# Kernel optimization log

Measured on AMD Instinct MI355X. Metric: run time of the kernel, lower is better.

## Reference

```python
import jax, jax.numpy as jnp
import numpy as np

B, C, S = 4, 2, 4096          # batch, in_channels, samples
K, NK, OUT = 64, 32, 512      # kernel_size, num_kernels, out_channels


def setup_inputs() -> dict:
    key = jax.random.key(0)
    k1, k2, k3, k4 = jax.random.split(key, 4)
    x = jax.random.normal(k1, (B, C, S), dtype=jnp.float32)
    # LearnableSTFTFunction.learnable_weights: (num_kernels, kernel_size), torch.randn init
    stft_w = jax.random.normal(k2, (NK, K), dtype=jnp.float32)
    # Conv1d(in=C*K*NK, out=OUT, kernel=1): weight (OUT, C*K*NK), bias (OUT,)
    conv_w = jax.random.normal(k3, (OUT, C * K * NK), dtype=jnp.float32) * 0.02
    conv_b = jax.random.normal(k4, (OUT,), dtype=jnp.float32) * 0.02
    return {"x": x, "stft_w": stft_w, "conv_w": conv_w, "conv_b": conv_b}


def reference(x, stft_w, conv_w, conv_b):
    b, c, s = x.shape
    nk, k = stft_w.shape
    # F.pad(x, (0, K-1)) then unfold(-1, K, 1) -> (b, c, s, K) sliding windows
    xp = jnp.pad(x, ((0, 0), (0, 0), (0, k - 1)))
    idx = jnp.arange(s)[:, None] + jnp.arange(k)[None, :]  # (s, K)
    win = xp[:, :, idx]  # (b, c, s, K)
    # einsum('ijklm,lm->ijkml') with l=1 broadcast: elementwise per-kernel weighting,
    # no reduction over m -> (b, c, s, K, NK)
    xw = jnp.einsum('bcsm,lm->bcsml', win, stft_w)
    # torch raw reshape (row-major), deliberately mixing s into channel blocks
    xr = xw.reshape(b, c * k * nk, s)
    # 1x1 Conv1d == channel matmul, then ReLU
    out = jnp.einsum('bis,oi->bos', xr, conv_w) + conv_b[None, :, None]
    return jax.nn.relu(out)
```

## Files before the change

kernel.cpp:

```cpp
#include <hip/hip_runtime.h>
#include <hip/hip_bf16.h>

#define NB   4
#define NC   2
#define NS   4096
#define NOUT 512
#define UPAD 80

typedef short  short8_t  __attribute__((ext_vector_type(8)));
typedef short  short4_t  __attribute__((ext_vector_type(4)));
typedef float  float16_t __attribute__((ext_vector_type(16)));

__device__ __forceinline__ short bf16s(float f) {
    union { __hip_bfloat16 b; short s; } u;
    u.b = __float2bfloat16(f);
    return u.s;
}
__device__ __forceinline__ float s2f(unsigned short s) {
    union { unsigned int u; float f; } v;
    v.u = ((unsigned int)s) << 16;
    return v.f;
}

template<int KCN>
__global__ __launch_bounds__(256)
void gemm_partials(const float* __restrict__ x,
                   const float* __restrict__ conv_w,
                   unsigned short* __restrict__ hpart)
{
    constexpr int KC      = 4096 / KCN;
    constexpr int XSZ     = KC + 56;
    constexpr int ASTRIDE = KC + 8;
    static_assert(KCN >= 8, "A-tile LDS exceeds 160KB below KCN=8");

    __shared__ __align__(16) short aS[128 * ASTRIDE];
    __shared__ __align__(16) short xS[16][XSZ];

    const int blk = blockIdx.x;
    const int kc  = blk % KCN;
    const int ot  = (blk / KCN) & 3;
    const int b   = blk / (KCN * 4);

    const int K0 = kc * KC;
    const int c  = K0 >> 11;
    const int tb = K0 & 2047;
    const int tid = threadIdx.x;

    const float* xc = x + (size_t)(b * NC + c) * NS;
    for (int i = tid; i < XSZ; i += 256) {
        int ge = (tb + i) * 2;
        float fe = (ge     < NS) ? xc[ge]     : 0.0f;
        float fo = (ge + 1 < NS) ? xc[ge + 1] : 0.0f;
        short se = bf16s(fe), so = bf16s(fo);
        #pragma unroll
        for (int r = 0; r < 8; ++r) {
            int j = i - r;
            if (j >= 0) { xS[r][j] = se; xS[8 + r][j] = so; }
        }
    }

    {
        const int rr = tid >> 5;
        const int cc = (tid & 31) * 4;
        const float* wbase = conv_w + (size_t)(ot * 128) * 4096 + K0;
        #pragma unroll
        for (int cb = 0; cb < KC; cb += 128) {
            #pragma unroll
            for (int it = 0; it < 16; ++it) {
                int row = it * 8 + rr;
                float4 v = *(const float4*)(wbase + (size_t)row * 4096 + cb + cc);
                short4_t p = { bf16s(v.x), bf16s(v.y), bf16s(v.z), bf16s(v.w) };
                *(short4_t*)&aS[row * ASTRIDE + cb + cc] = p;
            }
        }
    }
    __syncthreads();

    const int wave = tid >> 6;
    const int lane = tid & 63;
    const int l31  = lane & 31;
    const int q    = lane >> 5;

    const short* arow = &aS[(wave * 32 + l31) * ASTRIDE];

    float16_t acc[3];
    #pragma unroll
    for (int nt = 0; nt < 3; ++nt)
        #pragma unroll
        for (int e = 0; e < 16; ++e) acc[nt][e] = 0.0f;

    int arr[3], hb[3];
    #pragma unroll
    for (int nt = 0; nt < 3; ++nt) {
        int uu = nt * 32 + l31;
        int h  = uu >> 1;
        arr[nt] = (uu & 1) * 8 + (h & 7);
        hb[nt]  = h & ~7;
    }

    #pragma unroll
    for (int step = 0; step < KC / 16; ++step) {
        const int kl = step * 16 + q * 8;
        short8_t af = *(const short8_t*)(arow + kl);
        #pragma unroll
        for (int nt = 0; nt < 3; ++nt) {
            short8_t bf = *(const short8_t*)&xS[arr[nt]][kl + hb[nt]];
            acc[nt] = __builtin_amdgcn_mfma_f32_32x32x16_bf16(af, bf, acc[nt], 0, 0, 0);
        }
    }

    unsigned short* hp = hpart + (size_t)(kc * NB + b) * NOUT * UPAD;
    #pragma unroll
    for (int nt = 0; nt < 3; ++nt) {
        int uu = nt * 32 + l31;
        if (uu < UPAD) {
            #pragma unroll
            for (int reg = 0; reg < 16; ++reg) {
                int row = (reg & 3) + 8 * (reg >> 2) + 4 * q;
                int o   = ot * 128 + wave * 32 + row;
                hp[(size_t)o * UPAD + uu] = (unsigned short)bf16s(acc[nt][reg]);
            }
        }
    }
}

template<int KCN>
__global__ __launch_bounds__(256)
void reduce_epilogue(const unsigned short* __restrict__ hpart,
                     const float* __restrict__ stft_w,
                     const float* __restrict__ conv_b,
                     float* __restrict__ out)
{
    __shared__ float HsA[65], HsB[65];
    const int tid = threadIdx.x;
    const int bid = blockIdx.x;
    const int b = bid >> 9;
    const int o = bid & 511;

    constexpr int HALF = KCN / 2;
    const size_t slice = (size_t)NB * NOUT * UPAD;

    if (tid < 65) {
        const unsigned short* hp0 = hpart + ((size_t)b * NOUT + o) * UPAD + tid;
        float h = 0.0f;
        #pragma unroll
        for (int s = 0; s < HALF; ++s) h += s2f(hp0[(size_t)s * slice]);
        HsA[tid] = h;
    } else if (tid >= 128 && tid < 193) {
        const unsigned short* hp0 = hpart + ((size_t)b * NOUT + o) * UPAD + (tid - 128)
                                  + (size_t)HALF * slice;
        float h = 0.0f;
        #pragma unroll
        for (int s = 0; s < KCN - HALF; ++s) h += s2f(hp0[(size_t)s * slice]);
        HsB[tid - 128] = h;
    }
    __syncthreads();

    const float bias = conv_b[o];
    float* ob = out + (size_t)(b * NOUT + o) * NS;
    #pragma unroll
    for (int it = 0; it < 4; ++it) {
        int s4 = (it * 256 + tid) * 4;
        int r  = s4 >> 11;
        int qq = s4 & 2047;
        int m  = qq >> 5;
        int l  = qq & 31;
        float h = HsA[r + m] + HsB[r + m];
        float v0 = fmaf(stft_w[(l + 0) * 64 + m], h, bias);
        float v1 = fmaf(stft_w[(l + 1) * 64 + m], h, bias);
        float v2 = fmaf(stft_w[(l + 2) * 64 + m], h, bias);
        float v3 = fmaf(stft_w[(l + 3) * 64 + m], h, bias);
        float4 res;
        res.x = v0 > 0.0f ? v0 : 0.0f;
        res.y = v1 > 0.0f ? v1 : 0.0f;
        res.z = v2 > 0.0f ? v2 : 0.0f;
        res.w = v3 > 0.0f ? v3 : 0.0f;
        *(float4*)(ob + s4) = res;
    }
}

__device__ __forceinline__ int swz(int i) { return i + (i >> 5); }

__global__ __launch_bounds__(256, 3)
void fused_cnn(const float* __restrict__ x,
               const float* __restrict__ stft_w,
               const float* __restrict__ conv_w,
               const float* __restrict__ conv_b,
               float* __restrict__ out)
{
    __shared__ float xs[2 * 4290];
    __shared__ float ws_[4224];
    __shared__ float Hs[65];

    const int tid = threadIdx.x;
    const int bid = blockIdx.x;
    const int b = bid >> 9;
    const int o = bid & 511;

    for (int c = 0; c < NC; ++c) {
        const float* xb = x + (size_t)(b * NC + c) * NS;
        float* dst = xs + c * 4290;
        #pragma unroll
        for (int it = 0; it < 4; ++it) {
            int i0 = (it * 256 + tid) * 4;
            float4 v = *(const float4*)(xb + i0);
            dst[swz(i0 + 0)] = v.x; dst[swz(i0 + 1)] = v.y;
            dst[swz(i0 + 2)] = v.z; dst[swz(i0 + 3)] = v.w;
        }
        if (tid < 64) dst[swz(4096 + tid)] = 0.0f;
    }
    {
        const float* wrow = conv_w + (size_t)o * 4096;
        #pragma unroll
        for (int it = 0; it < 4; ++it) {
            int i0 = (it * 256 + tid) * 4;
            float4 v = *(const float4*)(wrow + i0);
            ws_[swz(i0 + 0)] = v.x; ws_[swz(i0 + 1)] = v.y;
            ws_[swz(i0 + 2)] = v.z; ws_[swz(i0 + 3)] = v.w;
        }
    }
    __syncthreads();

    const int wave = tid >> 6;
    const int lane = tid & 63;
    const int u0 = wave << 4;

    float acc[17];
    #pragma unroll
    for (int i = 0; i < 17; ++i) acc[i] = 0.0f;

    for (int g = 0; g < 8; ++g) {
        int G = lane + (g << 6);
        int c = G >> 8;
        int t0 = (G & 255) << 3;
        int wb = c * 2048 + t0;
        float w[8];
        #pragma unroll
        for (int j = 0; j < 8; ++j) w[j] = ws_[swz(wb + j)];
        const float* xcs = xs + c * 4290;
        int xb0 = 2 * t0 + u0;
        #pragma unroll
        for (int d = 0; d <= 30; ++d) {
            float xv = xcs[swz(xb0 + d)];
            #pragma unroll
            for (int j = 0; j < 8; ++j) {
                int uu = d - 2 * j;
                if (uu >= 0 && uu < 17) acc[uu] += w[j] * xv;
            }
        }
    }
    #pragma unroll
    for (int uu = 0; uu < 17; ++uu) {
        float v = acc[uu];
        #pragma unroll
        for (int off = 1; off < 64; off <<= 1) v += __shfl_xor(v, off, 64);
        acc[uu] = v;
    }
    if (lane == 0)
        #pragma unroll
        for (int uu = 0; uu < 17; ++uu)
            if (uu < 16 || wave == 3) Hs[u0 + uu] = acc[uu];
    __syncthreads();

    const float bias = conv_b[o];
    float* ob = out + (size_t)(b * NOUT + o) * NS;
    #pragma unroll
    for (int it = 0; it < 4; ++it) {
        int s4 = (it * 256 + tid) * 4;
        int r = s4 >> 11;
        int qq = s4 & 2047;
        int m = qq >> 5;
        int l = qq & 31;
        float h = Hs[r + m];
        float v0 = fmaf(stft_w[(l + 0) * 64 + m], h, bias);
        float v1 = fmaf(stft_w[(l + 1) * 64 + m], h, bias);
        float v2 = fmaf(stft_w[(l + 2) * 64 + m], h, bias);
        float v3 = fmaf(stft_w[(l + 3) * 64 + m], h, bias);
        float4 res;
        res.x = v0 > 0.0f ? v0 : 0.0f;
        res.y = v1 > 0.0f ? v1 : 0.0f;
        res.z = v2 > 0.0f ? v2 : 0.0f;
        res.w = v3 > 0.0f ? v3 : 0.0f;
        *(float4*)(ob + s4) = res;
    }
}

template<int KCN>
static void launch_pair(const float* x, const float* stft_w, const float* conv_w,
                        const float* conv_b, float* out, unsigned short* ws,
                        hipStream_t stream)
{
    gemm_partials<KCN><<<dim3(NB * 4 * KCN), dim3(256), 0, stream>>>(x, conv_w, ws);
    reduce_epilogue<KCN><<<dim3(NB * NOUT), dim3(256), 0, stream>>>(ws, stft_w, conv_b, out);
}

extern "C" void kernel_launch(void* const* d_in, const int* in_sizes, int n_in,
                              void* d_out, int out_size, void* d_ws, size_t ws_size,
                              hipStream_t stream) {
    const float* x      = (const float*)d_in[0];
    const float* stft_w = (const float*)d_in[1];
    const float* conv_w = (const float*)d_in[2];
    const float* conv_b = (const float*)d_in[3];
    float* out = (float*)d_out;
    unsigned short* ws = (unsigned short*)d_ws;

    const size_t per_slice = (size_t)NB * NOUT * UPAD * sizeof(unsigned short);
    if      (ws_size >= 32 * per_slice) launch_pair<32>(x, stft_w, conv_w, conv_b, out, ws, stream);
    else if (ws_size >= 16 * per_slice) launch_pair<16>(x, stft_w, conv_w, conv_b, out, ws, stream);
    else if (ws_size >=  8 * per_slice) launch_pair<8 >(x, stft_w, conv_w, conv_b, out, ws, stream);
    else
        fused_cnn<<<dim3(NB * NOUT), dim3(256), 0, stream>>>(x, stft_w, conv_w, conv_b, out);
}
```

Baseline: 88.28 us.

## Fuse split-K GEMM and reduce epilogue into one launch with a grid barrier

Merges the partial-GEMM kernel and the reduce/epilogue kernel into a single 512-block kernel. An atomic counter acts as a grid-wide barrier, and after it each block reduces and writes four (b,o) output rows. The goal is to save the second kernel launch and its gap. The trade-offs are an extra memset, a spin-wait that can deadlock unless all 512 blocks are co-resident (hence launch_bounds 256,2), and only 512 blocks for the epilogue instead of 2048.

```diff
diff --git a/kernel.cpp b/kernel.cpp
--- a/kernel.cpp
+++ b/kernel.cpp
@@ -6,6 +6,11 @@
 #define NS   4096
 #define NOUT 512
 #define UPAD 80
+#define KCN  32
+#define KC   128
+#define NBLK 512
+#define PART_BYTES ((size_t)KCN * NB * NOUT * UPAD * 2)
+#define CNT_OFF    PART_BYTES
 
 typedef short  short8_t  __attribute__((ext_vector_type(8)));
 typedef short  short4_t  __attribute__((ext_vector_type(4)));
@@ -22,24 +27,26 @@
     return v.f;
 }
 
-template<int KCN>
-__global__ __launch_bounds__(256)
-void gemm_partials(const float* __restrict__ x,
-                   const float* __restrict__ conv_w,
-                   unsigned short* __restrict__ hpart)
+__global__ __launch_bounds__(256, 2)
+void fused_onelaunch(const float* __restrict__ x,
+                     const float* __restrict__ stft_w,
+                     const float* __restrict__ conv_w,
+                     const float* __restrict__ conv_b,
+                     float* __restrict__ out,
+                     unsigned short* __restrict__ hpart,
+                     unsigned int* __restrict__ cnt)
 {
-    constexpr int KC      = 4096 / KCN;
     constexpr int XSZ     = KC + 56;
     constexpr int ASTRIDE = KC + 8;
-    static_assert(KCN >= 8, "A-tile LDS exceeds 160KB below KCN=8");
 
     __shared__ __align__(16) short aS[128 * ASTRIDE];
     __shared__ __align__(16) short xS[16][XSZ];
+    __shared__ float HsA[65], HsB[65];
 
     const int blk = blockIdx.x;
-    const int kc  = blk % KCN;
-    const int ot  = (blk / KCN) & 3;
-    const int b   = blk / (KCN * 4);
+    const int kc  = blk & 31;
+    const int ot  = (blk >> 5) & 3;
+    const int b   = blk >> 7;
 
     const int K0 = kc * KC;
     const int c  = K0 >> 11;
@@ -64,14 +71,11 @@
         const int cc = (tid & 31) * 4;
         const float* wbase = conv_w + (size_t)(ot * 128) * 4096 + K0;
         #pragma unroll
-        for (int cb = 0; cb < KC; cb += 128) {
-            #pragma unroll
-            for (int it = 0; it < 16; ++it) {
-                int row = it * 8 + rr;
-                float4 v = *(const float4*)(wbase + (size_t)row * 4096 + cb + cc);
-                short4_t p = { bf16s(v.x), bf16s(v.y), bf16s(v.z), bf16s(v.w) };
-                *(short4_t*)&aS[row * ASTRIDE + cb + cc] = p;
-            }
+        for (int it = 0; it < 16; ++it) {
+            int row = it * 8 + rr;
+            float4 v = *(const float4*)(wbase + (size_t)row * 4096 + cc);
+            short4_t p = { bf16s(v.x), bf16s(v.y), bf16s(v.z), bf16s(v.w) };
+            *(short4_t*)&aS[row * ASTRIDE + cc] = p;
         }
     }
     __syncthreads();
@@ -122,60 +126,64 @@
             }
         }
     }
-}
-
-template<int KCN>
-__global__ __launch_bounds__(256)
-void reduce_epilogue(const unsigned short* __restrict__ hpart,
-                     const float* __restrict__ stft_w,
-                     const float* __restrict__ conv_b,
-                     float* __restrict__ out)
-{
-    __shared__ float HsA[65], HsB[65];
-    const int tid = threadIdx.x;
-    const int bid = blockIdx.x;
-    const int b = bid >> 9;
-    const int o = bid & 511;
+
+    __syncthreads();
+    if (tid == 0) {
+        __threadfence();
+        atomicAdd(cnt, 1u);
+        while (__hip_atomic_load(cnt, __ATOMIC_ACQUIRE,
+                                 __HIP_MEMORY_SCOPE_AGENT) < NBLK)
+            __builtin_amdgcn_s_sleep(2);
+    }
+    __syncthreads();
+    __threadfence();
 
     constexpr int HALF = KCN / 2;
     const size_t slice = (size_t)NB * NOUT * UPAD;
 
-    if (tid < 65) {
-        const unsigned short* hp0 = hpart + ((size_t)b * NOUT + o) * UPAD + tid;
-        float h = 0.0f;
-        #pragma unroll
-        for (int s = 0; s < HALF; ++s) h += s2f(hp0[(size_t)s * slice]);
-        HsA[tid] = h;
-    } else if (tid >= 128 && tid < 193) {
-        const unsigned short* hp0 = hpart + ((size_t)b * NOUT + o) * UPAD + (tid - 128)
-                                  + (size_t)HALF * slice;
-        float h = 0.0f;
-        #pragma unroll
-        for (int s = 0; s < KCN - HALF; ++s) h += s2f(hp0[(size_t)s * slice]);
-        HsB[tid - 128] = h;
-    }
-    __syncthreads();
-
-    const float bias = conv_b[o];
-    float* ob = out + (size_t)(b * NOUT + o) * NS;
-    #pragma unroll
-    for (int it = 0; it < 4; ++it) {
-        int s4 = (it * 256 + tid) * 4;
-        int r  = s4 >> 11;
-        int qq = s4 & 2047;
-        int m  = qq >> 5;
-        int l  = qq & 31;
-        float h = HsA[r + m] + HsB[r + m];
-        float v0 = fmaf(stft_w[(l + 0) * 64 + m], h, bias);
-        float v1 = fmaf(stft_w[(l + 1) * 64 + m], h, bias);
-        float v2 = fmaf(stft_w[(l + 2) * 64 + m], h, bias);
-        float v3 = fmaf(stft_w[(l + 3) * 64 + m], h, bias);
-        float4 res;
-        res.x = v0 > 0.0f ? v0 : 0.0f;
-        res.y = v1 > 0.0f ? v1 : 0.0f;
-        res.z = v2 > 0.0f ? v2 : 0.0f;
-        res.w = v3 > 0.0f ? v3 : 0.0f;
-        *(float4*)(ob + s4) = res;
+    for (int i = 0; i < 4; ++i) {
+        const int P  = (blk << 2) + i;
+        const int b2 = P >> 9;
+        const int o2 = P & 511;
+
+        if (tid < 65) {
+            const unsigned short* hp0 = hpart + ((size_t)b2 * NOUT + o2) * UPAD + tid;
+            float h = 0.0f;
+            #pragma unroll
+            for (int s = 0; s < HALF; ++s) h += s2f(hp0[(size_t)s * slice]);
+            HsA[tid] = h;
+        } else if (tid >= 128 && tid < 193) {
+            const unsigned short* hp0 = hpart + ((size_t)b2 * NOUT + o2) * UPAD
+                                      + (tid - 128) + (size_t)HALF * slice;
+            float h = 0.0f;
+            #pragma unroll
+            for (int s = 0; s < KCN - HALF; ++s) h += s2f(hp0[(size_t)s * slice]);
+            HsB[tid - 128] = h;
+        }
+        __syncthreads();
+
+        const float bias = conv_b[o2];
+        float* ob = out + (size_t)(b2 * NOUT + o2) * NS;
+        #pragma unroll
+        for (int it = 0; it < 4; ++it) {
+            int s4 = (it * 256 + tid) * 4;
+            int r  = s4 >> 11;
+            int qq = s4 & 2047;
+            int m  = qq >> 5;
+            int l  = qq & 31;
+            float h = HsA[r + m] + HsB[r + m];
+            float v0 = fmaf(stft_w[(l + 0) * 64 + m], h, bias);
+            float v1 = fmaf(stft_w[(l + 1) * 64 + m], h, bias);
+            float v2 = fmaf(stft_w[(l + 2) * 64 + m], h, bias);
+            float v3 = fmaf(stft_w[(l + 3) * 64 + m], h, bias);
+            float4 res;
+            res.x = v0 > 0.0f ? v0 : 0.0f;
+            res.y = v1 > 0.0f ? v1 : 0.0f;
+            res.z = v2 > 0.0f ? v2 : 0.0f;
+            res.w = v3 > 0.0f ? v3 : 0.0f;
+            *(float4*)(ob + s4) = res;
+        }
+        __syncthreads();
     }
 }
 
@@ -285,15 +293,6 @@
     }
 }
 
-template<int KCN>
-static void launch_pair(const float* x, const float* stft_w, const float* conv_w,
-                        const float* conv_b, float* out, unsigned short* ws,
-                        hipStream_t stream)
-{
-    gemm_partials<KCN><<<dim3(NB * 4 * KCN), dim3(256), 0, stream>>>(x, conv_w, ws);
-    reduce_epilogue<KCN><<<dim3(NB * NOUT), dim3(256), 0, stream>>>(ws, stft_w, conv_b, out);
-}
-
 extern "C" void kernel_launch(void* const* d_in, const int* in_sizes, int n_in,
                               void* d_out, int out_size, void* d_ws, size_t ws_size,
                               hipStream_t stream) {
@@ -302,12 +301,15 @@
     const float* conv_w = (const float*)d_in[2];
     const float* conv_b = (const float*)d_in[3];
     float* out = (float*)d_out;
-    unsigned short* ws = (unsigned short*)d_ws;
-
-    const size_t per_slice = (size_t)NB * NOUT * UPAD * sizeof(unsigned short);
-    if      (ws_size >= 32 * per_slice) launch_pair<32>(x, stft_w, conv_w, conv_b, out, ws, stream);
-    else if (ws_size >= 16 * per_slice) launch_pair<16>(x, stft_w, conv_w, conv_b, out, ws, stream);
-    else if (ws_size >=  8 * per_slice) launch_pair<8 >(x, stft_w, conv_w, conv_b, out, ws, stream);
-    else
-        fused_cnn<<<dim3(NB * NOUT), dim3(256), 0, stream>>>(x, stft_w, conv_w, conv_b, out);
-}
+
+    if (ws_size >= CNT_OFF + 64) {
+        unsigned short* hpart = (unsigned short*)d_ws;
+        unsigned int*   cnt   = (unsigned int*)((char*)d_ws + CNT_OFF);
+        hipMemsetAsync((void*)cnt, 0, 4, stream);
+        fused_onelaunch<<<dim3(NBLK), dim3(256), 0, stream>>>(
+            x, stft_w, conv_w, conv_b, out, hpart, cnt);
+    } else {
+        fused_cnn<<<dim3(NB * NOUT), dim3(256), 0, stream>>>(
+            x, stft_w, conv_w, conv_b, out);
+    }
+}
```

Result: slower. 177.5 us (+101.1%).
